# Optimization experiments

Measured on AMD Instinct MI355X. Metric: run time of the kernel, lower is better.

## Reference

```python
import jax, jax.numpy as jnp
import numpy as np

N, F, H, E, ES, G = 50000, 64, 4, 300000, 400000, 128
NS, EPS = 0.2, 1e-5  # LeakyReLU slope, BN eps


def setup_inputs() -> dict:
    k = jax.random.split(jax.random.key(0), 16)
    rn = lambda i, s, sc=1.0: jax.random.normal(k[i], s, jnp.float32) * sc
    return {
        "x": rn(0, (N, F)),
        "edge_index": jax.random.randint(k[1], (2, E), 0, N),
        "batch": jnp.sort(jax.random.randint(k[2], (N,), 0, G)),
        "scatter_edge_index": jax.random.randint(k[3], (4, 2, ES), 0, N),
        "scatter_edge_attr": rn(4, (4, ES), 0.1),
        "gat_W": rn(5, (4, F, H * F), 0.05),
        "gat_asrc": rn(6, (4, H, F), 0.05),
        "gat_adst": rn(7, (4, H, F), 0.05),
        "gat_bias": jnp.zeros((4, H * F)),
        "mlp_W": rn(8, (4, H * F, F), 0.05),
        "mlp_b": jnp.zeros((4, F)),
        "mlp_g": jnp.ones((4, F)), "mlp_beta": jnp.zeros((4, F)),
        "mlp_rm": jnp.zeros((4, F)), "mlp_rv": jax.random.uniform(k[9], (4, F)) + 0.5,
        "fc1_W": rn(10, (F, 256), 0.05), "fc1_b": jnp.zeros((256,)),
        "fc1_g": jnp.ones((256,)), "fc1_beta": jnp.zeros((256,)),
        "fc1_rm": jnp.zeros((256,)), "fc1_rv": jax.random.uniform(k[11], (256,)) + 0.5,
        "fc2_W": rn(12, (256, 64), 0.05), "fc2_b": jnp.zeros((64,)),
        "fc2_g": jnp.ones((64,)), "fc2_beta": jnp.zeros((64,)),
        "fc2_rm": jnp.zeros((64,)), "fc2_rv": jax.random.uniform(k[13], (64,)) + 0.5,
        "fc3_W": rn(14, (64, 10), 0.05), "fc3_b": jnp.zeros((10,)),
        "fc3_g": jnp.ones((10,)), "fc3_beta": jnp.zeros((10,)),
        "fc3_rm": jnp.zeros((10,)), "fc3_rv": jax.random.uniform(k[15], (10,)) + 0.5,
    }


def _bn(h, g, b, rm, rv):
    # BatchNorm1d in eval mode (running stats)
    return g * (h - rm) * jax.lax.rsqrt(rv + EPS) + b


def _forward(floats, ints):
    (x, sea, gW, gas, gad, gb, mW, mb, mg, mbe, mrm, mrv,
     f1W, f1b, f1g, f1be, f1rm, f1rv, f2W, f2b, f2g, f2be, f2rm, f2rv,
     f3W, f3b, f3g, f3be, f3rm, f3rv) = floats
    edge_index, batch, sei = ints
    n = x.shape[0]
    loop = jnp.arange(n)
    src = jnp.concatenate([edge_index[0], loop])  # GATConv adds self-loops
    dst = jnp.concatenate([edge_index[1], loop])

    def solo(i, h):
        # edge_attr-weighted scatter-add (solo_pass, aggr='add')
        s, t = sei[i, 0], sei[i, 1]
        return jax.ops.segment_sum(sea[i][:, None] * h[s], t, num_segments=n)

    def gat_mlp(i, h):
        hh = (h @ gW[i]).reshape(n, H, F)                       # [N,H,F]
        e = (hh * gas[i]).sum(-1)[src] + (hh * gad[i]).sum(-1)[dst]  # [E+N,H]
        e = jnp.where(e > 0, e, NS * e)                         # LeakyReLU(0.2)
        m = jax.ops.segment_max(e, dst, num_segments=n)         # segment softmax over dst
        ex = jnp.exp(e - m[dst])
        ssum = jax.ops.segment_sum(ex, dst, num_segments=n)
        alpha = ex / ssum[dst]
        out = jax.ops.segment_sum(hh[src] * alpha[:, :, None], dst, num_segments=n)
        out = out.reshape(n, H * F) + gb[i]                     # concat heads + bias
        h2 = jax.nn.elu(out) @ mW[i] + mb[i]                    # ELU -> Dropout(eval) -> Linear
        return _bn(h2, mg[i], mbe[i], mrm[i], mrv[i])

    x0 = solo(0, x)
    xh = [jnp.abs(solo(i, x)) for i in (1, 2, 3)]
    branches = [x0] + [solo(0, h) for h in xh]
    branches = [gat_mlp(i, branches[i]) for i in range(4)]
    x_stage2 = x + branches[0] + branches[1] + branches[2] + branches[3]
    pooled = jax.ops.segment_sum(x_stage2, batch, num_segments=G)   # global_add_pool
    h = jax.nn.relu(_bn(pooled @ f1W + f1b, f1g, f1be, f1rm, f1rv))
    h = jax.nn.relu(_bn(h @ f2W + f2b, f2g, f2be, f2rm, f2rv))
    return _bn(h @ f3W + f3b, f3g, f3be, f3rm, f3rv)  # [G, num_classes]


def reference(x, edge_index, batch, scatter_edge_index, scatter_edge_attr, gat_W, gat_asrc, gat_adst, gat_bias, mlp_W, mlp_b, mlp_g, mlp_beta, mlp_rm, mlp_rv, fc1_W, fc1_b, fc1_g, fc1_beta, fc1_rm, fc1_rv, fc2_W, fc2_b, fc2_g, fc2_beta, fc2_rm, fc2_rv, fc3_W, fc3_b, fc3_g, fc3_beta, fc3_rm, fc3_rv):
    floats = (x, scatter_edge_attr, gat_W, gat_asrc, gat_adst, gat_bias, mlp_W, mlp_b, mlp_g, mlp_beta, mlp_rm, mlp_rv, fc1_W, fc1_b, fc1_g, fc1_beta, fc1_rm, fc1_rv, fc2_W, fc2_b, fc2_g, fc2_beta, fc2_rm, fc2_rv, fc3_W, fc3_b, fc3_g, fc3_beta, fc3_rm, fc3_rv)
    return _forward(floats, (edge_index, batch, scatter_edge_index))
```

## Files before the change

### kernel.cpp

```cpp
#include <hip/hip_runtime.h>

typedef unsigned int uint;
typedef unsigned short u16;

#define NN 50000
#define FF 64
#define NHD 4
#define EE 300000
#define ESN 400000
#define NG 128
#define NSLOPE 0.2f
#define EPSBN 1e-5f

#define BINSZ 64
#define NBIN 782
#define NPOS (NBIN * BINSZ)
#define CHUNK 2048
#define NBLK 196
#define BST 40
#define BCAP 38

typedef float f32x4 __attribute__((ext_vector_type(4)));
typedef float f32x2 __attribute__((ext_vector_type(2)));
typedef short bf16x8 __attribute__((ext_vector_type(8)));
// ... 248 lines not shown
    uint p5 = (j + 5 < deg) ? pc.y : 0u;
    uint p6 = (j + 6 < deg) ? pd.x : 0u;
    uint p7 = (j + 7 < deg) ? pd.y : 0u;
    uint4 v0 = *(const uint4*)&xbf[(size_t)(p0 & 0xFFFFu) * 32 + sl * 4];
    uint4 v1 = *(const uint4*)&xbf[(size_t)(p1 & 0xFFFFu) * 32 + sl * 4];
    uint4 v2 = *(const uint4*)&xbf[(size_t)(p2 & 0xFFFFu) * 32 + sl * 4];
    uint4 v3 = *(const uint4*)&xbf[(size_t)(p3 & 0xFFFFu) * 32 + sl * 4];
    uint4 v4 = *(const uint4*)&xbf[(size_t)(p4 & 0xFFFFu) * 32 + sl * 4];
    uint4 v5 = *(const uint4*)&xbf[(size_t)(p5 & 0xFFFFu) * 32 + sl * 4];
    uint4 v6 = *(const uint4*)&xbf[(size_t)(p6 & 0xFFFFu) * 32 + sl * 4];
    uint4 v7 = *(const uint4*)&xbf[(size_t)(p7 & 0xFFFFu) * 32 + sl * 4];
#define SOLOA_EDGE(V, W)                              \
    {                                                 \
      float w_ = (W);                                 \
      f32x2 w2_ = {w_, w_};                           \
      A0 += (f32x2){bl(V.x), bh(V.x)} * w2_;          \
      A1 += (f32x2){bl(V.y), bh(V.y)} * w2_;          \
      A2 += (f32x2){bl(V.z), bh(V.z)} * w2_;          \
      A3 += (f32x2){bl(V.w), bh(V.w)} * w2_;          \
    }
    SOLOA_EDGE(v0, bh(p0));
    SOLOA_EDGE(v1, bh(p1));
    SOLOA_EDGE(v2, bh(p2));
    SOLOA_EDGE(v3, bh(p3));
    SOLOA_EDGE(v4, bh(p4));
    SOLOA_EDGE(v5, bh(p5));
    SOLOA_EDGE(v6, bh(p6));
    SOLOA_EDGE(v7, bh(p7));
#undef SOLOA_EDGE
  }
  uint4 o;
  o.x = packbf(A0[0], A0[1]); o.y = packbf(A1[0], A1[1]);
  o.z = packbf(A2[0], A2[1]); o.w = packbf(A3[0], A3[1]);
  uint* out = (i == 0) ? bbuf : (tmpb + (size_t)(i - 1) * NN * 32);
  *(uint4*)&out[(size_t)id * 32 + sl * 4] = o;
  if (i == 0) {
    float pv[8] = {A0[0], A0[1], A1[0], A1[1], A2[0], A2[1], A3[0], A3[1]};
    const float* wa = wasd;
    float r[8];
#pragma unroll
    for (int o8 = 0; o8 < 8; ++o8) {
      const float* w8 = wa + o8 * 64 + sl * 8;
      float a = 0.f;
#pragma unroll
      for (int j = 0; j < 8; ++j) a += pv[j] * w8[j];
      r[o8] = a;
    }
#pragma unroll
    for (int off = 1; off < 8; off <<= 1)
#pragma unroll
      for (int o8 = 0; o8 < 8; ++o8) r[o8] += __shfl_xor(r[o8], off);
    if (sl == 0) {
      *(float4*)&es4[(size_t)id * 4] = make_float4(r[0], r[1], r[2], r[3]);
      *(float4*)&ed4[(size_t)id * 4] = make_float4(r[4], r[5], r[6], r[7]);
    }
  }
}

__global__ __launch_bounds__(256) void k_solo_gB(
    const uint* __restrict__ tmpb, const uint* __restrict__ pbk,
    const float* __restrict__ wasd, uint* __restrict__ bbuf,
    float* __restrict__ es4, float* __restrict__ ed4) {
  int tid = threadIdx.x;
  int pos = blockIdx.x * 32 + (tid >> 3);
  int sl = tid & 7;
  const uint* bk = pbk + (size_t)pos * BST;
  int deg = (int)bk[0]; deg = deg > BCAP ? BCAP : deg;
  int id = (int)bk[1];
  if (id >= NN) return;
  const uint* pp = bk + 2;
  const uint* t0 = tmpb;
  const uint* t1 = tmpb + (size_t)NN * 32;
  const uint* t2 = tmpb + (size_t)2 * NN * 32;
  f32x2 A[3][4];
#pragma unroll
  for (int k = 0; k < 3; ++k)
#pragma unroll
    for (int c = 0; c < 4; ++c) A[k][c] = (f32x2){0.f, 0.f};
  for (int j = 0; j < deg; j += 4) {
    uint2 pa = *(const uint2*)&pp[j];
    uint2 pb = *(const uint2*)&pp[j + 2];
    uint p0 = pa.x;
    uint p1 = (j + 1 < deg) ? pa.y : 0u;
    uint p2 = (j + 2 < deg) ? pb.x : 0u;
    uint p3 = (j + 3 < deg) ? pb.y : 0u;
    size_t ro0 = (size_t)(p0 & 0xFFFFu) * 32 + sl * 4;
    size_t ro1 = (size_t)(p1 & 0xFFFFu) * 32 + sl * 4;
    size_t ro2 = (size_t)(p2 & 0xFFFFu) * 32 + sl * 4;
    size_t ro3 = (size_t)(p3 & 0xFFFFu) * 32 + sl * 4;
    uint4 v00 = *(const uint4*)&t0[ro0];
    uint4 v01 = *(const uint4*)&t1[ro0];
    uint4 v02 = *(const uint4*)&t2[ro0];
    uint4 v10 = *(const uint4*)&t0[ro1];
    uint4 v11 = *(const uint4*)&t1[ro1];
    uint4 v12 = *(const uint4*)&t2[ro1];
    uint4 v20 = *(const uint4*)&t0[ro2];
    uint4 v21 = *(const uint4*)&t1[ro2];
    uint4 v22 = *(const uint4*)&t2[ro2];
    uint4 v30 = *(const uint4*)&t0[ro3];
    uint4 v31 = *(const uint4*)&t1[ro3];
    uint4 v32 = *(const uint4*)&t2[ro3];
    float w0 = bh(p0), w1 = bh(p1), w2 = bh(p2), w3 = bh(p3);
    f32x2 w20 = {w0, w0}, w21 = {w1, w1}, w22 = {w2, w2}, w23 = {w3, w3};
#define SOLOB_EDGE(K, V, W)                                       \
    {                                                             \
      A[K][0] += (f32x2){fabsf(bl(V.x)), fabsf(bh(V.x))} * (W);   \
      A[K][1] += (f32x2){fabsf(bl(V.y)), fabsf(bh(V.y))} * (W);   \
      A[K][2] += (f32x2){fabsf(bl(V.z)), fabsf(bh(V.z))} * (W);   \
      A[K][3] += (f32x2){fabsf(bl(V.w)), fabsf(bh(V.w))} * (W);   \
    }
    SOLOB_EDGE(0, v00, w20); SOLOB_EDGE(1, v01, w20); SOLOB_EDGE(2, v02, w20);
    SOLOB_EDGE(0, v10, w21); SOLOB_EDGE(1, v11, w21); SOLOB_EDGE(2, v12, w21);
    SOLOB_EDGE(0, v20, w22); SOLOB_EDGE(1, v21, w22); SOLOB_EDGE(2, v22, w22);
    SOLOB_EDGE(0, v30, w23); SOLOB_EDGE(1, v31, w23); SOLOB_EDGE(2, v32, w23);
#undef SOLOB_EDGE
  }
#pragma unroll
  for (int k = 0; k < 3; ++k) {
    int b = k + 1;
    uint4 o;
    o.x = packbf(A[k][0][0], A[k][0][1]); o.y = packbf(A[k][1][0], A[k][1][1]);
    o.z = packbf(A[k][2][0], A[k][2][1]); o.w = packbf(A[k][3][0], A[k][3][1]);
    *(uint4*)&bbuf[(size_t)b * NN * 32 + (size_t)id * 32 + sl * 4] = o;
    float pv[8] = {A[k][0][0], A[k][0][1], A[k][1][0], A[k][1][1],
                   A[k][2][0], A[k][2][1], A[k][3][0], A[k][3][1]};
    const float* wa = wasd + b * 512;
    float r[8];
#pragma unroll
    for (int o8 = 0; o8 < 8; ++o8) {
      const float* w8 = wa + o8 * 64 + sl * 8;
      float a = 0.f;
#pragma unroll
      for (int j = 0; j < 8; ++j) a += pv[j] * w8[j];
      r[o8] = a;
    }
#pragma unroll
    for (int off = 1; off < 8; off <<= 1)
#pragma unroll
      for (int o8 = 0; o8 < 8; ++o8) r[o8] += __shfl_xor(r[o8], off);
    if (sl == 0) {
      *(float4*)&es4[(size_t)b * NN * 4 + (size_t)id * 4] =
          make_float4(r[0], r[1], r[2], r[3]);
      *(float4*)&ed4[(size_t)b * NN * 4 + (size_t)id * 4] =
          make_float4(r[4], r[5], r[6], r[7]);
    }
  }
}

__global__ __launch_bounds__(256) void k_agg(
    const uint* __restrict__ gbk, const float* __restrict__ es4,
    const float* __restrict__ ed4, const uint* __restrict__ bbuf,
    uint* __restrict__ agg4) {
  __shared__ uint gbr[32][40];
  __shared__ uint2 meta[32][32];
  int br = blockIdx.y;
  const float4* es44 = (const float4*)(es4 + (size_t)br * NN * 4);
  const float4* ed44 = (const float4*)(ed4 + (size_t)br * NN * 4);
  const uint* bbf = bbuf + (size_t)br * NN * 32;
  int tid = threadIdx.x;
  int p0 = blockIdx.x * 32;
  for (int idx = tid; idx < 320; idx += 256) {
    int i = idx / 10, q = idx % 10;
    *(uint4*)&gbr[i][q * 4] =
        *(const uint4*)&gbk[((size_t)p0 + i) * BST + q * 4];
  }
  __syncthreads();
  {
    int g = tid >> 5, hl = tid & 31;
#pragma unroll
    for (int rep = 0; rep < 4; ++rep) {
      int i = rep * 8 + g;
      int id = (int)gbr[i][1];
      bool vld = id < NN;
      int nds = vld ? id : 0;
      int deg = vld ? (int)gbr[i][0] : 0;
      deg = deg > 31 ? 31 : deg;
      int s0 = (hl < deg) ? (int)gbr[i][2 + hl] : nds;
      bool act = hl <= deg;
      float4 edd = ed44[nds];
      float4 e4 = es44[s0];
      float val[4];
      val[0] = act ? lrelu(e4.x + edd.x) : -3e38f;
      val[1] = act ? lrelu(e4.y + edd.y) : -3e38f;
      val[2] = act ? lrelu(e4.z + edd.z) : -3e38f;
      val[3] = act ? lrelu(e4.w + edd.w) : -3e38f;
      float m[4] = {val[0], val[1], val[2], val[3]};
#pragma unroll
      for (int off = 1; off < 32; off <<= 1)
#pragma unroll
        for (int h = 0; h < 4; ++h) m[h] = fmaxf(m[h], __shfl_xor(m[h], off));
      float e[4], sm[4];
#pragma unroll
      for (int h = 0; h < 4; ++h) {
        e[h] = act ? __expf(val[h] - m[h]) : 0.f;
        sm[h] = e[h];
      }
#pragma unroll
      for (int off = 1; off < 32; off <<= 1)
#pragma unroll
        for (int h = 0; h < 4; ++h) sm[h] += __shfl_xor(sm[h], off);
      float inv[4];
#pragma unroll
      for (int h = 0; h < 4; ++h) inv[h] = __builtin_amdgcn_rcpf(sm[h]);
      meta[i][hl] = make_uint2(packbf(e[0] * inv[0], e[1] * inv[1]),
                               packbf(e[2] * inv[2], e[3] * inv[3]));
    }
  }
  __syncthreads();
  {
    int wv = tid >> 6, l = tid & 63;
    int i = wv * 8 + (l >> 3), sl = l & 7;
    int id = (int)gbr[i][1];
    bool vld = id < NN;
    int self = vld ? id : 0;
    int deg = vld ? (int)gbr[i][0] : 0;
    deg = deg > 31 ? 31 : deg;
    int tot = deg + 1;
    f32x2 a00={0.f,0.f},a01={0.f,0.f},a02={0.f,0.f},a03={0.f,0.f};
    f32x2 a10={0.f,0.f},a11={0.f,0.f},a12={0.f,0.f},a13={0.f,0.f};
    f32x2 a20={0.f,0.f},a21={0.f,0.f},a22={0.f,0.f},a23={0.f,0.f};
    f32x2 a30={0.f,0.f},a31={0.f,0.f},a32={0.f,0.f},a33={0.f,0.f};
    for (int j = 0; j < tot; j += 4) {
      int s0 = (j     < deg) ? (int)gbr[i][2 + j]  : self;
      int s1 = (j + 1 < deg) ? (int)gbr[i][3 + j]  : self;
      int s2 = (j + 2 < deg) ? (int)gbr[i][4 + j]  : self;
      int s3 = (j + 3 < deg) ? (int)gbr[i][5 + j]  : self;
      uint2 al0 = meta[i][j];
      uint2 al1 = meta[i][j + 1];
      uint2 al2 = meta[i][j + 2];
      uint2 al3 = meta[i][j + 3];
      uint4 v0 = *(const uint4*)&bbf[(size_t)s0 * 32 + sl * 4];
      uint4 v1 = *(const uint4*)&bbf[(size_t)s1 * 32 + sl * 4];
      uint4 v2 = *(const uint4*)&bbf[(size_t)s2 * 32 + sl * 4];
      uint4 v3 = *(const uint4*)&bbf[(size_t)s3 * 32 + sl * 4];
#define AGG_EDGE(V, AL)                                              \
      {                                                              \
        f32x2 w0_={bl(AL.x),bl(AL.x)}, w1_={bh(AL.x),bh(AL.x)};      \
        f32x2 w2_={bl(AL.y),bl(AL.y)}, w3_={bh(AL.y),bh(AL.y)};      \
        f32x2 p0_={bl(V.x),bh(V.x)}, p1_={bl(V.y),bh(V.y)};          \
        f32x2 p2_={bl(V.z),bh(V.z)}, p3_={bl(V.w),bh(V.w)};          \
        a00+=p0_*w0_; a01+=p1_*w0_; a02+=p2_*w0_; a03+=p3_*w0_;      \
        a10+=p0_*w1_; a11+=p1_*w1_; a12+=p2_*w1_; a13+=p3_*w1_;      \
        a20+=p0_*w2_; a21+=p1_*w2_; a22+=p2_*w2_; a23+=p3_*w2_;      \
        a30+=p0_*w3_; a31+=p1_*w3_; a32+=p2_*w3_; a33+=p3_*w3_;      \
      }
      AGG_EDGE(v0, al0);
      AGG_EDGE(v1, al1);
      AGG_EDGE(v2, al2);
      AGG_EDGE(v3, al3);
#undef AGG_EDGE
    }
    if (vld) {
      uint* outp = agg4 + ((size_t)br * NN + id) * 128;
      uint4 o;
      o.x=packbf(a00[0],a00[1]); o.y=packbf(a01[0],a01[1]);
      o.z=packbf(a02[0],a02[1]); o.w=packbf(a03[0],a03[1]);
      *(uint4*)&outp[0 * 32 + sl * 4] = o;
      o.x=packbf(a10[0],a10[1]); o.y=packbf(a11[0],a11[1]);
      o.z=packbf(a12[0],a12[1]); o.w=packbf(a13[0],a13[1]);
      *(uint4*)&outp[1 * 32 + sl * 4] = o;
      o.x=packbf(a20[0],a20[1]); o.y=packbf(a21[0],a21[1]);
      o.z=packbf(a22[0],a22[1]); o.w=packbf(a23[0],a23[1]);
      *(uint4*)&outp[2 * 32 + sl * 4] = o;
      o.x=packbf(a30[0],a30[1]); o.y=packbf(a31[0],a31[1]);
      o.z=packbf(a32[0],a32[1]); o.w=packbf(a33[0],a33[1]);
      *(uint4*)&outp[3 * 32 + sl * 4] = o;
    }
  }
}

__global__ __launch_bounds__(256) void k_mlp2(
    const uint* __restrict__ agg4, const uint* __restrict__ WB2,
    const uint* __restrict__ MB4, const float* __restrict__ gb,
    const float* __restrict__ cvec, const float* __restrict__ xsrc,
    float* __restrict__ xs2) {
  __shared__ union UU2 {
    struct {
      uint astg[32][128];
      uint elu[4][32][32];
    } s;
    float red[4][32][64];
  } u;
  int tid = threadIdx.x, wv = tid >> 6, l = tid & 63;
  int quad = l >> 4, m16 = l & 15;
  int n0 = blockIdx.x * 32;
  int h = wv;
  f32x4 macc[2][4] = {{{0.f,0.f,0.f,0.f},{0.f,0.f,0.f,0.f},
                       {0.f,0.f,0.f,0.f},{0.f,0.f,0.f,0.f}},
                      {{0.f,0.f,0.f,0.f},{0.f,0.f,0.f,0.f},
                       {0.f,0.f,0.f,0.f},{0.f,0.f,0.f,0.f}}};
  u16* eluw = (u16*)&u.s.elu[wv][0][0];
  for (int br = 0; br < 4; ++br) {
    if (br) __syncthreads();
    {
      const uint* src = agg4 + ((size_t)br * NN + n0) * 128;
      for (int i2 = tid; i2 < 4096; i2 += 256) {
        int row = i2 >> 7, col = i2 & 127;
        u.s.astg[row][col ^ ((row & 7) << 2)] = src[i2];
      }
    }
    __syncthreads();
    uint4 Bh[2][4];
#pragma unroll
    for (int kk = 0; kk < 2; ++kk)
#pragma unroll
      for (int ct = 0; ct < 4; ++ct)
        Bh[kk][ct] =
            ((const uint4*)WB2)[(((br * 4 + h) * 2 + kk) * 4 + ct) * 64 + l];
#pragma unroll
    for (int mt = 0; mt < 2; ++mt) {
      int row = mt * 16 + m16;
      const uint* ar = &u.s.astg[row][0];
      int sw = (row & 7) << 2;
      U8 a0, a1;
      a0.u = *(const uint4*)&ar[(h * 32 + quad * 4) ^ sw];
      a1.u = *(const uint4*)&ar[(h * 32 + 16 + quad * 4) ^ sw];
#pragma unroll
      for (int ct = 0; ct < 4; ++ct) {
        f32x4 acc = {0.f, 0.f, 0.f, 0.f};
        U8 b0, b1; b0.u = Bh[0][ct]; b1.u = Bh[1][ct];
        acc = __builtin_amdgcn_mfma_f32_16x16x32_bf16(a0.s, b0.s, acc, 0, 0, 0);
        acc = __builtin_amdgcn_mfma_f32_16x16x32_bf16(a1.s, b1.s, acc, 0, 0, 0);
        float gbv = gb[br * 256 + h * 64 + ct * 16 + m16];
#pragma unroll
        for (int r = 0; r < 4; ++r) {
          float v = acc[r] + gbv;
          v = v > 0.f ? v : (__expf(v) - 1.f);
          int erow = mt * 16 + quad * 4 + r;
          int ucs = ((ct * 16 + m16) >> 1) ^ ((erow & 7) << 2);
          eluw[(erow * 32 + ucs) * 2 + (m16 & 1)] = (u16)f2bf(v);
        }
      }
    }
    const uint4* MBb = (const uint4*)MB4 + br * 2048;
    uint4 Bm[4][2];
#pragma unroll
    for (int t = 0; t < 4; ++t)
#pragma unroll
      for (int kk = 0; kk < 2; ++kk)
        Bm[t][kk] = MBb[(t * 8 + wv * 2 + kk) * 64 + l];
#pragma unroll
    for (int mt = 0; mt < 2; ++mt) {
      int row = mt * 16 + m16;
      int sw = (row & 7) << 2;
      const uint* er = &u.s.elu[wv][row][0];
      U8 a0, a1;
      a0.u = *(const uint4*)&er[(quad * 4) ^ sw];
      a1.u = *(const uint4*)&er[(16 + quad * 4) ^ sw];
#pragma unroll
      for (int t = 0; t < 4; ++t) {
        U8 b0, b1; b0.u = Bm[t][0]; b1.u = Bm[t][1];
        macc[mt][t] =
            __builtin_amdgcn_mfma_f32_16x16x32_bf16(a0.s, b0.s, macc[mt][t], 0, 0, 0);
        macc[mt][t] =
            __builtin_amdgcn_mfma_f32_16x16x32_bf16(a1.s, b1.s, macc[mt][t], 0, 0, 0);
      }
    }
  }
  __syncthreads();
#pragma unroll
  for (int mt = 0; mt < 2; ++mt)
#pragma unroll
    for (int t = 0; t < 4; ++t)
#pragma unroll
      for (int r = 0; r < 4; ++r)
        u.red[wv][mt * 16 + quad * 4 + r][t * 16 + m16] = macc[mt][t][r];
  __syncthreads();
  for (int e = tid; e < 2048; e += 256) {
    int node = e >> 6, col = e & 63;
    int nd = n0 + node;
    if (nd < NN) {
      float v = u.red[0][node][col] + u.red[1][node][col] +
                u.red[2][node][col] + u.red[3][node][col];
      size_t idx = (size_t)nd * 64 + col;
      xs2[idx] = xsrc[idx] + v + cvec[col];
    }
  }
}

__global__ __launch_bounds__(256) void k_poolhead(
    const float* __restrict__ xs2, const int* __restrict__ batch,
    const float* __restrict__ f1W, const float* __restrict__ f1b,
    const float* __restrict__ f1g, const float* __restrict__ f1be,
    const float* __restrict__ f1rm, const float* __restrict__ f1rv,
    const float* __restrict__ f2W, const float* __restrict__ f2b,
    const float* __restrict__ f2g, const float* __restrict__ f2be,
    const float* __restrict__ f2rm, const float* __restrict__ f2rv,
    const float* __restrict__ f3W, const float* __restrict__ f3b,
    const float* __restrict__ f3g, const float* __restrict__ f3be,
    const float* __restrict__ f3rm, const float* __restrict__ f3rv,
    float* __restrict__ out) {
  __shared__ float p[64], h1[256], h2[64], red[4][64];
  int g = blockIdx.x, tid = threadIdx.x;
  int wv = tid >> 6, lane = tid & 63;
  int lo = 0, hi = NN;
  while (lo < hi) { int mid = (lo + hi) >> 1; if (batch[mid] < g) lo = mid + 1; else hi = mid; }
  int beg = lo;
  lo = 0; hi = NN;
  while (lo < hi) { int mid = (lo + hi) >> 1; if (batch[mid] < g + 1) lo = mid + 1; else hi = mid; }
  int end = lo;
  float acc = 0.f;
  for (int n = beg + wv; n < end; n += 4) acc += xs2[(size_t)n * FF + lane];
  red[wv][lane] = acc;
  __syncthreads();
  if (tid < 64) p[tid] = red[0][tid] + red[1][tid] + red[2][tid] + red[3][tid];
  __syncthreads();
  {
    float a = f1b[tid];
    for (int k = 0; k < 64; ++k) a += p[k] * f1W[k * 256 + tid];
    a = f1g[tid] * (a - f1rm[tid]) * rsqrtf(f1rv[tid] + EPSBN) + f1be[tid];
    h1[tid] = a > 0.f ? a : 0.f;
  }
  __syncthreads();
  if (tid < 64) {
    float b = f2b[tid];
    for (int k = 0; k < 256; ++k) b += h1[k] * f2W[k * 64 + tid];
    b = f2g[tid] * (b - f2rm[tid]) * rsqrtf(f2rv[tid] + EPSBN) + f2be[tid];
    h2[tid] = b > 0.f ? b : 0.f;
  }
  __syncthreads();
  if (tid < 10) {
    float c = f3b[tid];
    for (int k = 0; k < 64; ++k) c += h2[k] * f3W[k * 10 + tid];
    c = f3g[tid] * (c - f3rm[tid]) * rsqrtf(f3rv[tid] + EPSBN) + f3be[tid];
    out[g * 10 + tid] = c;
  }
}

extern "C" void kernel_launch(void* const* d_in, const int* in_sizes, int n_in,
                              void* d_out, int out_size, void* d_ws,
                              size_t ws_size, hipStream_t stream) {
  const float* x     = (const float*)d_in[0];
  const int*   ei    = (const int*)d_in[1];
  const int*   batch = (const int*)d_in[2];
  const int*   sei   = (const int*)d_in[3];
  const float* sea   = (const float*)d_in[4];
  const float* gW    = (const float*)d_in[5];
  const float* gas   = (const float*)d_in[6];
  const float* gad   = (const float*)d_in[7];
  const float* gb    = (const float*)d_in[8];
  const float* mW    = (const float*)d_in[9];
  const float* mb    = (const float*)d_in[10];
  const float* mg    = (const float*)d_in[11];
  const float* mbe   = (const float*)d_in[12];
  const float* mrm   = (const float*)d_in[13];
  const float* mrv   = (const float*)d_in[14];
  const float* f1W   = (const float*)d_in[15];
  const float* f1b   = (const float*)d_in[16];
  const float* f1g   = (const float*)d_in[17];
  const float* f1be  = (const float*)d_in[18];
  const float* f1rm  = (const float*)d_in[19];
  const float* f1rv  = (const float*)d_in[20];
  const float* f2W   = (const float*)d_in[21];
  const float* f2b   = (const float*)d_in[22];
  const float* f2g   = (const float*)d_in[23];
  const float* f2be  = (const float*)d_in[24];
  const float* f2rm  = (const float*)d_in[25];
  const float* f2rv  = (const float*)d_in[26];
  const float* f3W   = (const float*)d_in[27];
  const float* f3b   = (const float*)d_in[28];
  const float* f3g   = (const float*)d_in[29];
  const float* f3be  = (const float*)d_in[30];
  const float* f3rm  = (const float*)d_in[31];
  const float* f3rv  = (const float*)d_in[32];
  float* out = (float*)d_out;

  char* base = (char*)d_ws;
  float* xs2 = (float*)base;
  uint* gbk  = (uint*)(base + (size_t)NN * 64 * 4);
  uint* xbf  = gbk + (size_t)NPOS * BST;
  uint* bbuf = xbf + (size_t)NN * 32;
  uint* tmpb = bbuf + (size_t)4 * NN * 32;
  uint* pbk  = tmpb + (size_t)3 * NN * 32;
  uint2* sorted = (uint2*)(pbk + (size_t)4 * NPOS * BST);
  u16* offs = (u16*)(sorted + (size_t)5 * NBLK * CHUNK);
  uint* agg4 = (uint*)(offs + (size_t)5 * NBLK * 784);
  float* es4 = (float*)(agg4 + ((size_t)4 * NN + 32) * 128);
  float* ed4 = es4 + (size_t)4 * NN * 4;
  float* cvec = ed4 + (size_t)4 * NN * 4;
  float* wasd = cvec + 64;
  uint* WB2 = (uint*)(wasd + 2048);
  uint* MB4 = WB2 + 4 * 8192;

  size_t need = (size_t)((char*)(MB4 + 4 * 8192) - base);
  if (ws_size < need) return;

  k_setup<<<(NN * 32 + 255) / 256, 256, 0, stream>>>(
      (const float2*)x, gW, gas, gad, mW, mb, mg, mbe, mrm, mrv, xbf, WB2,
      wasd, MB4, cvec);

  dim3 gS1(NBLK, 5);
  k_sort1<<<gS1, 256, 0, stream>>>(sei, sea, ei, sorted, offs);
  dim3 gS2(NBIN, 5);
  k_sort2<<<gS2, 256, 0, stream>>>(offs, sorted, pbk, gbk);

  dim3 gA(NPOS / 32, 4);
  k_solo_gA<<<gA, 256, 0, stream>>>(xbf, pbk, wasd, bbuf, tmpb, es4, ed4);
  k_solo_gB<<<NPOS / 32, 256, 0, stream>>>(tmpb, pbk, wasd, bbuf, es4, ed4);

  dim3 gAg(NPOS / 32, 4);
  k_agg<<<gAg, 256, 0, stream>>>(gbk, es4, ed4, bbuf, agg4);
  k_mlp2<<<(NN + 31) / 32, 256, 0, stream>>>(agg4, WB2, MB4, gb, cvec, x, xs2);

  k_poolhead<<<NG, 256, 0, stream>>>(xs2, batch, f1W, f1b, f1g, f1be, f1rm,
                                     f1rv, f2W, f2b, f2g, f2be, f2rm, f2rv,
                                     f3W, f3b, f3g, f3be, f3rm, f3rv, out);
}
```

Before: 392.8 us.

## Fuse GAT aggregation with MLP, interleave tmp buffers, widen pool head

Merges the attention-aggregation kernel and the MLP kernel into one kernel. Each block loops over the four branches, aggregates into shared memory and feeds the MFMA MLP directly, so the bf16 agg4 intermediate no longer round-trips through global memory. The three solo temp buffers are interleaved per node (stride 96), so the gB gather reads contiguous memory per neighbour. The pool head moves to 512 threads. The cost is fewer parallel blocks for aggregation (no branch grid dimension), with the four branches now serialised inside each block, which may lower latency hiding.

```diff
diff --git a/kernel.cpp b/kernel.cpp
--- a/kernel.cpp
+++ b/kernel.cpp
@@ -304,8 +304,11 @@
   uint4 o;
   o.x = packbf(A0[0], A0[1]); o.y = packbf(A1[0], A1[1]);
   o.z = packbf(A2[0], A2[1]); o.w = packbf(A3[0], A3[1]);
-  uint* out = (i == 0) ? bbuf : (tmpb + (size_t)(i - 1) * NN * 32);
-  *(uint4*)&out[(size_t)id * 32 + sl * 4] = o;
+  if (i == 0) {
+    *(uint4*)&bbuf[(size_t)id * 32 + sl * 4] = o;
+  } else {
+    *(uint4*)&tmpb[(size_t)id * 96 + (size_t)(i - 1) * 32 + sl * 4] = o;
+  }
   if (i == 0) {
     float pv[8] = {A0[0], A0[1], A1[0], A1[1], A2[0], A2[1], A3[0], A3[1]};
     const float* wa = wasd;
@@ -341,9 +344,6 @@
   int id = (int)bk[1];
   if (id >= NN) return;
   const uint* pp = bk + 2;
-  const uint* t0 = tmpb;
-  const uint* t1 = tmpb + (size_t)NN * 32;
-  const uint* t2 = tmpb + (size_t)2 * NN * 32;
   f32x2 A[3][4];
 #pragma unroll
   for (int k = 0; k < 3; ++k)
@@ -356,22 +356,22 @@
     uint p1 = (j + 1 < deg) ? pa.y : 0u;
     uint p2 = (j + 2 < deg) ? pb.x : 0u;
     uint p3 = (j + 3 < deg) ? pb.y : 0u;
-    size_t ro0 = (size_t)(p0 & 0xFFFFu) * 32 + sl * 4;
-    size_t ro1 = (size_t)(p1 & 0xFFFFu) * 32 + sl * 4;
-    size_t ro2 = (size_t)(p2 & 0xFFFFu) * 32 + sl * 4;
-    size_t ro3 = (size_t)(p3 & 0xFFFFu) * 32 + sl * 4;
-    uint4 v00 = *(const uint4*)&t0[ro0];
-    uint4 v01 = *(const uint4*)&t1[ro0];
-    uint4 v02 = *(const uint4*)&t2[ro0];
-    uint4 v10 = *(const uint4*)&t0[ro1];
-    uint4 v11 = *(const uint4*)&t1[ro1];
-    uint4 v12 = *(const uint4*)&t2[ro1];
-    uint4 v20 = *(const uint4*)&t0[ro2];
-    uint4 v21 = *(const uint4*)&t1[ro2];
-    uint4 v22 = *(const uint4*)&t2[ro2];
-    uint4 v30 = *(const uint4*)&t0[ro3];
-    uint4 v31 = *(const uint4*)&t1[ro3];
-    uint4 v32 = *(const uint4*)&t2[ro3];
+    const uint* b0 = &tmpb[(size_t)(p0 & 0xFFFFu) * 96 + sl * 4];
+    const uint* b1 = &tmpb[(size_t)(p1 & 0xFFFFu) * 96 + sl * 4];
+    const uint* b2 = &tmpb[(size_t)(p2 & 0xFFFFu) * 96 + sl * 4];
+    const uint* b3 = &tmpb[(size_t)(p3 & 0xFFFFu) * 96 + sl * 4];
+    uint4 v00 = *(const uint4*)&b0[0];
+    uint4 v01 = *(const uint4*)&b0[32];
+    uint4 v02 = *(const uint4*)&b0[64];
+    uint4 v10 = *(const uint4*)&b1[0];
+    uint4 v11 = *(const uint4*)&b1[32];
+    uint4 v12 = *(const uint4*)&b1[64];
+    uint4 v20 = *(const uint4*)&b2[0];
+    uint4 v21 = *(const uint4*)&b2[32];
+    uint4 v22 = *(const uint4*)&b2[64];
+    uint4 v30 = *(const uint4*)&b3[0];
+    uint4 v31 = *(const uint4*)&b3[32];
+    uint4 v32 = *(const uint4*)&b3[64];
     float w0 = bh(p0), w1 = bh(p1), w2 = bh(p2), w3 = bh(p3);
     f32x2 w20 = {w0, w0}, w21 = {w1, w1}, w22 = {w2, w2}, w23 = {w3, w3};
 #define SOLOB_EDGE(K, V, W)                                       \
@@ -419,217 +419,200 @@
   }
 }
 
-__global__ __launch_bounds__(256) void k_agg(
+__global__ __launch_bounds__(256) void k_aggf(
     const uint* __restrict__ gbk, const float* __restrict__ es4,
     const float* __restrict__ ed4, const uint* __restrict__ bbuf,
-    uint* __restrict__ agg4) {
+    const uint* __restrict__ WB2, const uint* __restrict__ MB4,
+    const float* __restrict__ gb, const float* __restrict__ cvec,
+    const float* __restrict__ xsrc, float* __restrict__ xs2) {
   __shared__ uint gbr[32][40];
-  __shared__ uint2 meta[32][32];
-  int br = blockIdx.y;
-  const float4* es44 = (const float4*)(es4 + (size_t)br * NN * 4);
-  const float4* ed44 = (const float4*)(ed4 + (size_t)br * NN * 4);
-  const uint* bbf = bbuf + (size_t)br * NN * 32;
-  int tid = threadIdx.x;
+  __shared__ union UF {
+    struct { uint metaelu[4096]; uint astg[4096]; } s;
+    float red[4][32][64];
+  } u;
+  int tid = threadIdx.x, wv = tid >> 6, l = tid & 63;
+  int quad = l >> 4, m16 = l & 15;
   int p0 = blockIdx.x * 32;
   for (int idx = tid; idx < 320; idx += 256) {
     int i = idx / 10, q = idx % 10;
     *(uint4*)&gbr[i][q * 4] =
         *(const uint4*)&gbk[((size_t)p0 + i) * BST + q * 4];
   }
-  __syncthreads();
-  {
-    int g = tid >> 5, hl = tid & 31;
-#pragma unroll
-    for (int rep = 0; rep < 4; ++rep) {
-      int i = rep * 8 + g;
-      int id = (int)gbr[i][1];
-      bool vld = id < NN;
-      int nds = vld ? id : 0;
-      int deg = vld ? (int)gbr[i][0] : 0;
-      deg = deg > 31 ? 31 : deg;
-      int s0 = (hl < deg) ? (int)gbr[i][2 + hl] : nds;
-      bool act = hl <= deg;
-      float4 edd = ed44[nds];
-      float4 e4 = es44[s0];
-      float val[4];
-      val[0] = act ? lrelu(e4.x + edd.x) : -3e38f;
-      val[1] = act ? lrelu(e4.y + edd.y) : -3e38f;
-      val[2] = act ? lrelu(e4.z + edd.z) : -3e38f;
-      val[3] = act ? lrelu(e4.w + edd.w) : -3e38f;
-      float m[4] = {val[0], val[1], val[2], val[3]};
-#pragma unroll
-      for (int off = 1; off < 32; off <<= 1)
-#pragma unroll
-        for (int h = 0; h < 4; ++h) m[h] = fmaxf(m[h], __shfl_xor(m[h], off));
-      float e[4], sm[4];
-#pragma unroll
-      for (int h = 0; h < 4; ++h) {
-        e[h] = act ? __expf(val[h] - m[h]) : 0.f;
-        sm[h] = e[h];
-      }
-#pragma unroll
-      for (int off = 1; off < 32; off <<= 1)
-#pragma unroll
-        for (int h = 0; h < 4; ++h) sm[h] += __shfl_xor(sm[h], off);
-      float inv[4];
-#pragma unroll
-      for (int h = 0; h < 4; ++h) inv[h] = __builtin_amdgcn_rcpf(sm[h]);
-      meta[i][hl] = make_uint2(packbf(e[0] * inv[0], e[1] * inv[1]),
-                               packbf(e[2] * inv[2], e[3] * inv[3]));
-    }
-  }
-  __syncthreads();
-  {
-    int wv = tid >> 6, l = tid & 63;
-    int i = wv * 8 + (l >> 3), sl = l & 7;
-    int id = (int)gbr[i][1];
-    bool vld = id < NN;
-    int self = vld ? id : 0;
-    int deg = vld ? (int)gbr[i][0] : 0;
-    deg = deg > 31 ? 31 : deg;
-    int tot = deg + 1;
-    f32x2 a00={0.f,0.f},a01={0.f,0.f},a02={0.f,0.f},a03={0.f,0.f};
-    f32x2 a10={0.f,0.f},a11={0.f,0.f},a12={0.f,0.f},a13={0.f,0.f};
-    f32x2 a20={0.f,0.f},a21={0.f,0.f},a22={0.f,0.f},a23={0.f,0.f};
-    f32x2 a30={0.f,0.f},a31={0.f,0.f},a32={0.f,0.f},a33={0.f,0.f};
-    for (int j = 0; j < tot; j += 4) {
-      int s0 = (j     < deg) ? (int)gbr[i][2 + j]  : self;
-      int s1 = (j + 1 < deg) ? (int)gbr[i][3 + j]  : self;
-      int s2 = (j + 2 < deg) ? (int)gbr[i][4 + j]  : self;
-      int s3 = (j + 3 < deg) ? (int)gbr[i][5 + j]  : self;
-      uint2 al0 = meta[i][j];
-      uint2 al1 = meta[i][j + 1];
-      uint2 al2 = meta[i][j + 2];
-      uint2 al3 = meta[i][j + 3];
-      uint4 v0 = *(const uint4*)&bbf[(size_t)s0 * 32 + sl * 4];
-      uint4 v1 = *(const uint4*)&bbf[(size_t)s1 * 32 + sl * 4];
-      uint4 v2 = *(const uint4*)&bbf[(size_t)s2 * 32 + sl * 4];
-      uint4 v3 = *(const uint4*)&bbf[(size_t)s3 * 32 + sl * 4];
-#define AGG_EDGE(V, AL)                                              \
-      {                                                              \
-        f32x2 w0_={bl(AL.x),bl(AL.x)}, w1_={bh(AL.x),bh(AL.x)};      \
-        f32x2 w2_={bl(AL.y),bl(AL.y)}, w3_={bh(AL.y),bh(AL.y)};      \
-        f32x2 p0_={bl(V.x),bh(V.x)}, p1_={bl(V.y),bh(V.y)};          \
-        f32x2 p2_={bl(V.z),bh(V.z)}, p3_={bl(V.w),bh(V.w)};          \
-        a00+=p0_*w0_; a01+=p1_*w0_; a02+=p2_*w0_; a03+=p3_*w0_;      \
-        a10+=p0_*w1_; a11+=p1_*w1_; a12+=p2_*w1_; a13+=p3_*w1_;      \
-        a20+=p0_*w2_; a21+=p1_*w2_; a22+=p2_*w2_; a23+=p3_*w2_;      \
-        a30+=p0_*w3_; a31+=p1_*w3_; a32+=p2_*w3_; a33+=p3_*w3_;      \
-      }
-      AGG_EDGE(v0, al0);
-      AGG_EDGE(v1, al1);
-      AGG_EDGE(v2, al2);
-      AGG_EDGE(v3, al3);
-#undef AGG_EDGE
-    }
-    if (vld) {
-      uint* outp = agg4 + ((size_t)br * NN + id) * 128;
-      uint4 o;
-      o.x=packbf(a00[0],a00[1]); o.y=packbf(a01[0],a01[1]);
-      o.z=packbf(a02[0],a02[1]); o.w=packbf(a03[0],a03[1]);
-      *(uint4*)&outp[0 * 32 + sl * 4] = o;
-      o.x=packbf(a10[0],a10[1]); o.y=packbf(a11[0],a11[1]);
-      o.z=packbf(a12[0],a12[1]); o.w=packbf(a13[0],a13[1]);
-      *(uint4*)&outp[1 * 32 + sl * 4] = o;
-      o.x=packbf(a20[0],a20[1]); o.y=packbf(a21[0],a21[1]);
-      o.z=packbf(a22[0],a22[1]); o.w=packbf(a23[0],a23[1]);
-      *(uint4*)&outp[2 * 32 + sl * 4] = o;
-      o.x=packbf(a30[0],a30[1]); o.y=packbf(a31[0],a31[1]);
-      o.z=packbf(a32[0],a32[1]); o.w=packbf(a33[0],a33[1]);
-      *(uint4*)&outp[3 * 32 + sl * 4] = o;
-    }
-  }
-}
-
-__global__ __launch_bounds__(256) void k_mlp2(
-    const uint* __restrict__ agg4, const uint* __restrict__ WB2,
-    const uint* __restrict__ MB4, const float* __restrict__ gb,
-    const float* __restrict__ cvec, const float* __restrict__ xsrc,
-    float* __restrict__ xs2) {
-  __shared__ union UU2 {
-    struct {
-      uint astg[32][128];
-      uint elu[4][32][32];
-    } s;
-    float red[4][32][64];
-  } u;
-  int tid = threadIdx.x, wv = tid >> 6, l = tid & 63;
-  int quad = l >> 4, m16 = l & 15;
-  int n0 = blockIdx.x * 32;
-  int h = wv;
   f32x4 macc[2][4] = {{{0.f,0.f,0.f,0.f},{0.f,0.f,0.f,0.f},
                        {0.f,0.f,0.f,0.f},{0.f,0.f,0.f,0.f}},
                       {{0.f,0.f,0.f,0.f},{0.f,0.f,0.f,0.f},
                        {0.f,0.f,0.f,0.f},{0.f,0.f,0.f,0.f}}};
-  u16* eluw = (u16*)&u.s.elu[wv][0][0];
+  __syncthreads();
   for (int br = 0; br < 4; ++br) {
-    if (br) __syncthreads();
+    const float4* es44 = (const float4*)(es4 + (size_t)br * NN * 4);
+    const float4* ed44 = (const float4*)(ed4 + (size_t)br * NN * 4);
+    const uint* bbf = bbuf + (size_t)br * NN * 32;
     {
-      const uint* src = agg4 + ((size_t)br * NN + n0) * 128;
-      for (int i2 = tid; i2 < 4096; i2 += 256) {
-        int row = i2 >> 7, col = i2 & 127;
-        u.s.astg[row][col ^ ((row & 7) << 2)] = src[i2];
+      uint2* meta = (uint2*)u.s.metaelu;
+      int g = tid >> 5, hl = tid & 31;
+#pragma unroll
+      for (int rep = 0; rep < 4; ++rep) {
+        int i = rep * 8 + g;
+        int id = (int)gbr[i][1];
+        bool vld = id < NN;
+        int nds = vld ? id : 0;
+        int deg = vld ? (int)gbr[i][0] : 0;
+        deg = deg > 31 ? 31 : deg;
+        int s0 = (hl < deg) ? (int)gbr[i][2 + hl] : nds;
+        bool act = hl <= deg;
+        float4 edd = ed44[nds];
+        float4 e4 = es44[s0];
+        float val[4];
+        val[0] = act ? lrelu(e4.x + edd.x) : -3e38f;
+        val[1] = act ? lrelu(e4.y + edd.y) : -3e38f;
+        val[2] = act ? lrelu(e4.z + edd.z) : -3e38f;
+        val[3] = act ? lrelu(e4.w + edd.w) : -3e38f;
+        float m[4] = {val[0], val[1], val[2], val[3]};
+#pragma unroll
+        for (int off = 1; off < 32; off <<= 1)
+#pragma unroll
+          for (int h = 0; h < 4; ++h) m[h] = fmaxf(m[h], __shfl_xor(m[h], off));
+        float e[4], sm[4];
+#pragma unroll
+        for (int h = 0; h < 4; ++h) {
+          e[h] = act ? __expf(val[h] - m[h]) : 0.f;
+          sm[h] = e[h];
+        }
+#pragma unroll
+        for (int off = 1; off < 32; off <<= 1)
+#pragma unroll
+          for (int h = 0; h < 4; ++h) sm[h] += __shfl_xor(sm[h], off);
+        float inv[4];
+#pragma unroll
+        for (int h = 0; h < 4; ++h) inv[h] = __builtin_amdgcn_rcpf(sm[h]);
+        meta[i * 32 + hl] = make_uint2(packbf(e[0] * inv[0], e[1] * inv[1]),
+                                       packbf(e[2] * inv[2], e[3] * inv[3]));
       }
     }
     __syncthreads();
-    uint4 Bh[2][4];
-#pragma unroll
-    for (int kk = 0; kk < 2; ++kk)
-#pragma unroll
-      for (int ct = 0; ct < 4; ++ct)
-        Bh[kk][ct] =
-            ((const uint4*)WB2)[(((br * 4 + h) * 2 + kk) * 4 + ct) * 64 + l];
-#pragma unroll
-    for (int mt = 0; mt < 2; ++mt) {
-      int row = mt * 16 + m16;
-      const uint* ar = &u.s.astg[row][0];
-      int sw = (row & 7) << 2;
-      U8 a0, a1;
-      a0.u = *(const uint4*)&ar[(h * 32 + quad * 4) ^ sw];
-      a1.u = *(const uint4*)&ar[(h * 32 + 16 + quad * 4) ^ sw];
-#pragma unroll
-      for (int ct = 0; ct < 4; ++ct) {
-        f32x4 acc = {0.f, 0.f, 0.f, 0.f};
-        U8 b0, b1; b0.u = Bh[0][ct]; b1.u = Bh[1][ct];
-        acc = __builtin_amdgcn_mfma_f32_16x16x32_bf16(a0.s, b0.s, acc, 0, 0, 0);
-        acc = __builtin_amdgcn_mfma_f32_16x16x32_bf16(a1.s, b1.s, acc, 0, 0, 0);
-        float gbv = gb[br * 256 + h * 64 + ct * 16 + m16];
-#pragma unroll
-        for (int r = 0; r < 4; ++r) {
-          float v = acc[r] + gbv;
-          v = v > 0.f ? v : (__expf(v) - 1.f);
-          int erow = mt * 16 + quad * 4 + r;
-          int ucs = ((ct * 16 + m16) >> 1) ^ ((erow & 7) << 2);
-          eluw[(erow * 32 + ucs) * 2 + (m16 & 1)] = (u16)f2bf(v);
+    {
+      const uint2* meta = (const uint2*)u.s.metaelu;
+      int i = wv * 8 + (l >> 3), sl = l & 7;
+      int id = (int)gbr[i][1];
+      bool vld = id < NN;
+      int self = vld ? id : 0;
+      int deg = vld ? (int)gbr[i][0] : 0;
+      deg = deg > 31 ? 31 : deg;
+      int tot = deg + 1;
+      f32x2 a00={0.f,0.f},a01={0.f,0.f},a02={0.f,0.f},a03={0.f,0.f};
+      f32x2 a10={0.f,0.f},a11={0.f,0.f},a12={0.f,0.f},a13={0.f,0.f};
+      f32x2 a20={0.f,0.f},a21={0.f,0.f},a22={0.f,0.f},a23={0.f,0.f};
+      f32x2 a30={0.f,0.f},a31={0.f,0.f},a32={0.f,0.f},a33={0.f,0.f};
+      for (int j = 0; j < tot; j += 4) {
+        int s0 = (j     < deg) ? (int)gbr[i][2 + j]  : self;
+        int s1 = (j + 1 < deg) ? (int)gbr[i][3 + j]  : self;
+        int s2 = (j + 2 < deg) ? (int)gbr[i][4 + j]  : self;
+        int s3 = (j + 3 < deg) ? (int)gbr[i][5 + j]  : self;
+        uint2 al0 = meta[i * 32 + j];
+        uint2 al1 = meta[i * 32 + j + 1];
+        uint2 al2 = meta[i * 32 + j + 2];
+        uint2 al3 = meta[i * 32 + j + 3];
+        uint4 v0 = *(const uint4*)&bbf[(size_t)s0 * 32 + sl * 4];
+        uint4 v1 = *(const uint4*)&bbf[(size_t)s1 * 32 + sl * 4];
+        uint4 v2 = *(const uint4*)&bbf[(size_t)s2 * 32 + sl * 4];
+        uint4 v3 = *(const uint4*)&bbf[(size_t)s3 * 32 + sl * 4];
+#define AGG_EDGE(V, AL)                                              \
+        {                                                            \
+          f32x2 w0_={bl(AL.x),bl(AL.x)}, w1_={bh(AL.x),bh(AL.x)};    \
+          f32x2 w2_={bl(AL.y),bl(AL.y)}, w3_={bh(AL.y),bh(AL.y)};    \
+          f32x2 p0_={bl(V.x),bh(V.x)}, p1_={bl(V.y),bh(V.y)};        \
+          f32x2 p2_={bl(V.z),bh(V.z)}, p3_={bl(V.w),bh(V.w)};        \
+          a00+=p0_*w0_; a01+=p1_*w0_; a02+=p2_*w0_; a03+=p3_*w0_;    \
+          a10+=p0_*w1_; a11+=p1_*w1_; a12+=p2_*w1_; a13+=p3_*w1_;    \
+          a20+=p0_*w2_; a21+=p1_*w2_; a22+=p2_*w2_; a23+=p3_*w2_;    \
+          a30+=p0_*w3_; a31+=p1_*w3_; a32+=p2_*w3_; a33+=p3_*w3_;    \
+        }
+        AGG_EDGE(v0, al0);
+        AGG_EDGE(v1, al1);
+        AGG_EDGE(v2, al2);
+        AGG_EDGE(v3, al3);
+#undef AGG_EDGE
+      }
+      int swi = (i & 7) << 2;
+      uint4 o;
+      o.x=packbf(a00[0],a00[1]); o.y=packbf(a01[0],a01[1]);
+      o.z=packbf(a02[0],a02[1]); o.w=packbf(a03[0],a03[1]);
+      *(uint4*)&u.s.astg[i * 128 + ((0 * 32 + sl * 4) ^ swi)] = o;
+      o.x=packbf(a10[0],a10[1]); o.y=packbf(a11[0],a11[1]);
+      o.z=packbf(a12[0],a12[1]); o.w=packbf(a13[0],a13[1]);
+      *(uint4*)&u.s.astg[i * 128 + ((1 * 32 + sl * 4) ^ swi)] = o;
+      o.x=packbf(a20[0],a20[1]); o.y=packbf(a21[0],a21[1]);
+      o.z=packbf(a22[0],a22[1]); o.w=packbf(a23[0],a23[1]);
+      *(uint4*)&u.s.astg[i * 128 + ((2 * 32 + sl * 4) ^ swi)] = o;
+      o.x=packbf(a30[0],a30[1]); o.y=packbf(a31[0],a31[1]);
+      o.z=packbf(a32[0],a32[1]); o.w=packbf(a33[0],a33[1]);
+      *(uint4*)&u.s.astg[i * 128 + ((3 * 32 + sl * 4) ^ swi)] = o;
+    }
+    __syncthreads();
+    {
+      int h = wv;
+      u16* eluw = (u16*)&u.s.metaelu[wv * 1024];
+      uint4 Bh[2][4];
+#pragma unroll
+      for (int kk = 0; kk < 2; ++kk)
+#pragma unroll
+        for (int ct = 0; ct < 4; ++ct)
+          Bh[kk][ct] =
+              ((const uint4*)WB2)[(((br * 4 + h) * 2 + kk) * 4 + ct) * 64 + l];
+#pragma unroll
+      for (int mt = 0; mt < 2; ++mt) {
+        int row = mt * 16 + m16;
+        int sw = (row & 7) << 2;
+        U8 a0, a1;
+        a0.u = *(const uint4*)&u.s.astg[row * 128 + ((h * 32 + quad * 4) ^ sw)];
+        a1.u = *(const uint4*)&u.s.astg[row * 128 +
+                                        ((h * 32 + 16 + quad * 4) ^ sw)];
+#pragma unroll
+        for (int ct = 0; ct < 4; ++ct) {
+          f32x4 acc = {0.f, 0.f, 0.f, 0.f};
+          U8 b0, b1; b0.u = Bh[0][ct]; b1.u = Bh[1][ct];
+          acc = __builtin_amdgcn_mfma_f32_16x16x32_bf16(a0.s, b0.s, acc, 0, 0, 0);
+          acc = __builtin_amdgcn_mfma_f32_16x16x32_bf16(a1.s, b1.s, acc, 0, 0, 0);
+          float gbv = gb[br * 256 + h * 64 + ct * 16 + m16];
+#pragma unroll
+          for (int r = 0; r < 4; ++r) {
+            float v = acc[r] + gbv;
+            v = v > 0.f ? v : (__expf(v) - 1.f);
+            int erow = mt * 16 + quad * 4 + r;
+            int ucs = ((ct * 16 + m16) >> 1) ^ ((erow & 7) << 2);
+            eluw[(erow * 32 + ucs) * 2 + (m16 & 1)] = (u16)f2bf(v);
+          }
         }
       }
     }
-    const uint4* MBb = (const uint4*)MB4 + br * 2048;
-    uint4 Bm[4][2];
-#pragma unroll
-    for (int t = 0; t < 4; ++t)
-#pragma unroll
-      for (int kk = 0; kk < 2; ++kk)
-        Bm[t][kk] = MBb[(t * 8 + wv * 2 + kk) * 64 + l];
-#pragma unroll
-    for (int mt = 0; mt < 2; ++mt) {
-      int row = mt * 16 + m16;
-      int sw = (row & 7) << 2;
-      const uint* er = &u.s.elu[wv][row][0];
-      U8 a0, a1;
-      a0.u = *(const uint4*)&er[(quad * 4) ^ sw];
-      a1.u = *(const uint4*)&er[(16 + quad * 4) ^ sw];
-#pragma unroll
-      for (int t = 0; t < 4; ++t) {
-        U8 b0, b1; b0.u = Bm[t][0]; b1.u = Bm[t][1];
-        macc[mt][t] =
-            __builtin_amdgcn_mfma_f32_16x16x32_bf16(a0.s, b0.s, macc[mt][t], 0, 0, 0);
-        macc[mt][t] =
-            __builtin_amdgcn_mfma_f32_16x16x32_bf16(a1.s, b1.s, macc[mt][t], 0, 0, 0);
+    {
+      const uint4* MBb = (const uint4*)MB4 + br * 2048;
+      uint4 Bm[4][2];
+#pragma unroll
+      for (int t = 0; t < 4; ++t)
+#pragma unroll
+        for (int kk = 0; kk < 2; ++kk)
+          Bm[t][kk] = MBb[(t * 8 + wv * 2 + kk) * 64 + l];
+#pragma unroll
+      for (int mt = 0; mt < 2; ++mt) {
+        int row = mt * 16 + m16;
+        int sw = (row & 7) << 2;
+        const uint* er = &u.s.metaelu[wv * 1024 + row * 32];
+        U8 a0, a1;
+        a0.u = *(const uint4*)&er[(quad * 4) ^ sw];
+        a1.u = *(const uint4*)&er[(16 + quad * 4) ^ sw];
+#pragma unroll
+        for (int t = 0; t < 4; ++t) {
+          U8 b0, b1; b0.u = Bm[t][0]; b1.u = Bm[t][1];
+          macc[mt][t] =
+              __builtin_amdgcn_mfma_f32_16x16x32_bf16(a0.s, b0.s, macc[mt][t], 0, 0, 0);
+          macc[mt][t] =
+              __builtin_amdgcn_mfma_f32_16x16x32_bf16(a1.s, b1.s, macc[mt][t], 0, 0, 0);
+        }
       }
     }
-  }
-  __syncthreads();
+    __syncthreads();
+  }
 #pragma unroll
   for (int mt = 0; mt < 2; ++mt)
 #pragma unroll
@@ -640,17 +623,17 @@
   __syncthreads();
   for (int e = tid; e < 2048; e += 256) {
     int node = e >> 6, col = e & 63;
-    int nd = n0 + node;
-    if (nd < NN) {
+    int id = (int)gbr[node][1];
+    if (id < NN) {
       float v = u.red[0][node][col] + u.red[1][node][col] +
                 u.red[2][node][col] + u.red[3][node][col];
-      size_t idx = (size_t)nd * 64 + col;
+      size_t idx = (size_t)id * 64 + col;
       xs2[idx] = xsrc[idx] + v + cvec[col];
     }
   }
 }
 
-__global__ __launch_bounds__(256) void k_poolhead(
+__global__ __launch_bounds__(512) void k_poolhead(
     const float* __restrict__ xs2, const int* __restrict__ batch,
     const float* __restrict__ f1W, const float* __restrict__ f1b,
     const float* __restrict__ f1g, const float* __restrict__ f1be,
@@ -662,7 +645,7 @@
     const float* __restrict__ f3g, const float* __restrict__ f3be,
     const float* __restrict__ f3rm, const float* __restrict__ f3rv,
     float* __restrict__ out) {
-  __shared__ float p[64], h1[256], h2[64], red[4][64];
+  __shared__ float p[64], h1[256], h2[64], red[8][64];
   int g = blockIdx.x, tid = threadIdx.x;
   int wv = tid >> 6, lane = tid & 63;
   int lo = 0, hi = NN;
@@ -672,12 +655,17 @@
   while (lo < hi) { int mid = (lo + hi) >> 1; if (batch[mid] < g + 1) lo = mid + 1; else hi = mid; }
   int end = lo;
   float acc = 0.f;
-  for (int n = beg + wv; n < end; n += 4) acc += xs2[(size_t)n * FF + lane];
+  for (int n = beg + wv; n < end; n += 8) acc += xs2[(size_t)n * FF + lane];
   red[wv][lane] = acc;
   __syncthreads();
-  if (tid < 64) p[tid] = red[0][tid] + red[1][tid] + red[2][tid] + red[3][tid];
-  __syncthreads();
-  {
+  if (tid < 64) {
+    float s = 0.f;
+#pragma unroll
+    for (int w = 0; w < 8; ++w) s += red[w][tid];
+    p[tid] = s;
+  }
+  __syncthreads();
+  if (tid < 256) {
     float a = f1b[tid];
     for (int k = 0; k < 64; ++k) a += p[k] * f1W[k * 256 + tid];
     a = f1g[tid] * (a - f1rm[tid]) * rsqrtf(f1rv[tid] + EPSBN) + f1be[tid];
@@ -743,11 +731,10 @@
   uint* xbf  = gbk + (size_t)NPOS * BST;
   uint* bbuf = xbf + (size_t)NN * 32;
   uint* tmpb = bbuf + (size_t)4 * NN * 32;
-  uint* pbk  = tmpb + (size_t)3 * NN * 32;
+  uint* pbk  = tmpb + (size_t)NN * 96;
   uint2* sorted = (uint2*)(pbk + (size_t)4 * NPOS * BST);
   u16* offs = (u16*)(sorted + (size_t)5 * NBLK * CHUNK);
-  uint* agg4 = (uint*)(offs + (size_t)5 * NBLK * 784);
-  float* es4 = (float*)(agg4 + ((size_t)4 * NN + 32) * 128);
+  float* es4 = (float*)(offs + (size_t)5 * NBLK * 784);
   float* ed4 = es4 + (size_t)4 * NN * 4;
   float* cvec = ed4 + (size_t)4 * NN * 4;
   float* wasd = cvec + 64;
@@ -770,11 +757,10 @@
   k_solo_gA<<<gA, 256, 0, stream>>>(xbf, pbk, wasd, bbuf, tmpb, es4, ed4);
   k_solo_gB<<<NPOS / 32, 256, 0, stream>>>(tmpb, pbk, wasd, bbuf, es4, ed4);
 
-  dim3 gAg(NPOS / 32, 4);
-  k_agg<<<gAg, 256, 0, stream>>>(gbk, es4, ed4, bbuf, agg4);
-  k_mlp2<<<(NN + 31) / 32, 256, 0, stream>>>(agg4, WB2, MB4, gb, cvec, x, xs2);
-
-  k_poolhead<<<NG, 256, 0, stream>>>(xs2, batch, f1W, f1b, f1g, f1be, f1rm,
+  k_aggf<<<NPOS / 32, 256, 0, stream>>>(gbk, es4, ed4, bbuf, WB2, MB4, gb,
+                                        cvec, x, xs2);
+
+  k_poolhead<<<NG, 512, 0, stream>>>(xs2, batch, f1W, f1b, f1g, f1be, f1rm,
                                      f1rv, f2W, f2b, f2g, f2be, f2rm, f2rv,
                                      f3W, f3b, f3g, f3be, f3rm, f3rv, out);
 }
```

After: 426.3 us. 1.09x slower.

## Interleave three solo branch buffers per node and widen pooling head block

Applied to the files above, without the earlier changes.

The three intermediate bf16 solo outputs move from separate planes into one interleaved row of 96 words per node. Each gathered neighbour in k_solo_gB then reads one contiguous 384-byte span instead of three scattered rows, which improves cache-line locality for the random gather. Separately, k_poolhead now launches 512 threads, so eight waves share the global_add_pool segment reduction. This needs an extra guard for the fc1 stage and a larger shared reduction array.

```diff
diff --git a/kernel.cpp b/kernel.cpp
--- a/kernel.cpp
+++ b/kernel.cpp
@@ -304,8 +304,11 @@
   uint4 o;
   o.x = packbf(A0[0], A0[1]); o.y = packbf(A1[0], A1[1]);
   o.z = packbf(A2[0], A2[1]); o.w = packbf(A3[0], A3[1]);
-  uint* out = (i == 0) ? bbuf : (tmpb + (size_t)(i - 1) * NN * 32);
-  *(uint4*)&out[(size_t)id * 32 + sl * 4] = o;
+  if (i == 0) {
+    *(uint4*)&bbuf[(size_t)id * 32 + sl * 4] = o;
+  } else {
+    *(uint4*)&tmpb[(size_t)id * 96 + (size_t)(i - 1) * 32 + sl * 4] = o;
+  }
   if (i == 0) {
     float pv[8] = {A0[0], A0[1], A1[0], A1[1], A2[0], A2[1], A3[0], A3[1]};
     const float* wa = wasd;
@@ -341,9 +344,6 @@
   int id = (int)bk[1];
   if (id >= NN) return;
   const uint* pp = bk + 2;
-  const uint* t0 = tmpb;
-  const uint* t1 = tmpb + (size_t)NN * 32;
-  const uint* t2 = tmpb + (size_t)2 * NN * 32;
   f32x2 A[3][4];
 #pragma unroll
   for (int k = 0; k < 3; ++k)
@@ -356,22 +356,22 @@
     uint p1 = (j + 1 < deg) ? pa.y : 0u;
     uint p2 = (j + 2 < deg) ? pb.x : 0u;
     uint p3 = (j + 3 < deg) ? pb.y : 0u;
-    size_t ro0 = (size_t)(p0 & 0xFFFFu) * 32 + sl * 4;
-    size_t ro1 = (size_t)(p1 & 0xFFFFu) * 32 + sl * 4;
-    size_t ro2 = (size_t)(p2 & 0xFFFFu) * 32 + sl * 4;
-    size_t ro3 = (size_t)(p3 & 0xFFFFu) * 32 + sl * 4;
-    uint4 v00 = *(const uint4*)&t0[ro0];
-    uint4 v01 = *(const uint4*)&t1[ro0];
-    uint4 v02 = *(const uint4*)&t2[ro0];
-    uint4 v10 = *(const uint4*)&t0[ro1];
-    uint4 v11 = *(const uint4*)&t1[ro1];
-    uint4 v12 = *(const uint4*)&t2[ro1];
-    uint4 v20 = *(const uint4*)&t0[ro2];
-    uint4 v21 = *(const uint4*)&t1[ro2];
-    uint4 v22 = *(const uint4*)&t2[ro2];
-    uint4 v30 = *(const uint4*)&t0[ro3];
-    uint4 v31 = *(const uint4*)&t1[ro3];
-    uint4 v32 = *(const uint4*)&t2[ro3];
+    const uint* b0 = &tmpb[(size_t)(p0 & 0xFFFFu) * 96 + sl * 4];
+    const uint* b1 = &tmpb[(size_t)(p1 & 0xFFFFu) * 96 + sl * 4];
+    const uint* b2 = &tmpb[(size_t)(p2 & 0xFFFFu) * 96 + sl * 4];
+    const uint* b3 = &tmpb[(size_t)(p3 & 0xFFFFu) * 96 + sl * 4];
+    uint4 v00 = *(const uint4*)&b0[0];
+    uint4 v01 = *(const uint4*)&b0[32];
+    uint4 v02 = *(const uint4*)&b0[64];
+    uint4 v10 = *(const uint4*)&b1[0];
+    uint4 v11 = *(const uint4*)&b1[32];
+    uint4 v12 = *(const uint4*)&b1[64];
+    uint4 v20 = *(const uint4*)&b2[0];
+    uint4 v21 = *(const uint4*)&b2[32];
+    uint4 v22 = *(const uint4*)&b2[64];
+    uint4 v30 = *(const uint4*)&b3[0];
+    uint4 v31 = *(const uint4*)&b3[32];
+    uint4 v32 = *(const uint4*)&b3[64];
     float w0 = bh(p0), w1 = bh(p1), w2 = bh(p2), w3 = bh(p3);
     f32x2 w20 = {w0, w0}, w21 = {w1, w1}, w22 = {w2, w2}, w23 = {w3, w3};
 #define SOLOB_EDGE(K, V, W)                                       \
@@ -650,7 +650,7 @@
   }
 }
 
-__global__ __launch_bounds__(256) void k_poolhead(
+__global__ __launch_bounds__(512) void k_poolhead(
     const float* __restrict__ xs2, const int* __restrict__ batch,
     const float* __restrict__ f1W, const float* __restrict__ f1b,
     const float* __restrict__ f1g, const float* __restrict__ f1be,
@@ -662,7 +662,7 @@
     const float* __restrict__ f3g, const float* __restrict__ f3be,
     const float* __restrict__ f3rm, const float* __restrict__ f3rv,
     float* __restrict__ out) {
-  __shared__ float p[64], h1[256], h2[64], red[4][64];
+  __shared__ float p[64], h1[256], h2[64], red[8][64];
   int g = blockIdx.x, tid = threadIdx.x;
   int wv = tid >> 6, lane = tid & 63;
   int lo = 0, hi = NN;
@@ -672,12 +672,17 @@
   while (lo < hi) { int mid = (lo + hi) >> 1; if (batch[mid] < g + 1) lo = mid + 1; else hi = mid; }
   int end = lo;
   float acc = 0.f;
-  for (int n = beg + wv; n < end; n += 4) acc += xs2[(size_t)n * FF + lane];
+  for (int n = beg + wv; n < end; n += 8) acc += xs2[(size_t)n * FF + lane];
   red[wv][lane] = acc;
   __syncthreads();
-  if (tid < 64) p[tid] = red[0][tid] + red[1][tid] + red[2][tid] + red[3][tid];
-  __syncthreads();
-  {
+  if (tid < 64) {
+    float s = 0.f;
+#pragma unroll
+    for (int w = 0; w < 8; ++w) s += red[w][tid];
+    p[tid] = s;
+  }
+  __syncthreads();
+  if (tid < 256) {
     float a = f1b[tid];
     for (int k = 0; k < 64; ++k) a += p[k] * f1W[k * 256 + tid];
     a = f1g[tid] * (a - f1rm[tid]) * rsqrtf(f1rv[tid] + EPSBN) + f1be[tid];
@@ -743,7 +748,7 @@
   uint* xbf  = gbk + (size_t)NPOS * BST;
   uint* bbuf = xbf + (size_t)NN * 32;
   uint* tmpb = bbuf + (size_t)4 * NN * 32;
-  uint* pbk  = tmpb + (size_t)3 * NN * 32;
+  uint* pbk  = tmpb + (size_t)NN * 96;
   uint2* sorted = (uint2*)(pbk + (size_t)4 * NPOS * BST);
   u16* offs = (u16*)(sorted + (size_t)5 * NBLK * CHUNK);
   uint* agg4 = (uint*)(offs + (size_t)5 * NBLK * 784);
@@ -774,7 +779,7 @@
   k_agg<<<gAg, 256, 0, stream>>>(gbk, es4, ed4, bbuf, agg4);
   k_mlp2<<<(NN + 31) / 32, 256, 0, stream>>>(agg4, WB2, MB4, gb, cvec, x, xs2);
 
-  k_poolhead<<<NG, 256, 0, stream>>>(xs2, batch, f1W, f1b, f1g, f1be, f1rm,
+  k_poolhead<<<NG, 512, 0, stream>>>(xs2, batch, f1W, f1b, f1g, f1be, f1rm,
                                      f1rv, f2W, f2b, f2g, f2be, f2rm, f2rv,
                                      f3W, f3b, f3g, f3be, f3rm, f3rv, out);
 }
```

Measured after the change: 378.2 us. -3.7%, faster.
